# Performance work log

Measured on AMD Instinct MI355X. Metric: run time of the kernel, lower is better.

Reference implementation:

```python
import jax, jax.numpy as jnp
import numpy as np

VOCAB, EMB, UNITS, DENSE, B, T = 100, 10, 32, 25, 4096, 512

def setup_inputs() -> dict:
    key = jax.random.key(0)
    ks = jax.random.split(key, 7)
    inputs = jax.random.randint(ks[0], (B, T), 0, VOCAB, dtype=jnp.int32)
    emb = jax.random.normal(ks[1], (VOCAB, EMB), dtype=jnp.float32) * 0.05
    kernel = jax.random.normal(ks[2], (EMB, 3 * UNITS), dtype=jnp.float32) * 0.1
    rec_kernel = jax.random.normal(ks[3], (UNITS, 3 * UNITS), dtype=jnp.float32) * 0.1
    bias = jnp.zeros((2, 3 * UNITS), dtype=jnp.float32)  # [input_bias, recurrent_bias] (reset_after=True)
    dense_w = jax.random.normal(ks[4], (UNITS, DENSE), dtype=jnp.float32) * 0.1
    dense_b = jnp.zeros((DENSE,), dtype=jnp.float32)
    return {"inputs": inputs, "emb": emb, "kernel": kernel, "rec_kernel": rec_kernel,
            "bias": bias, "dense_w": dense_w, "dense_b": dense_b}

def _gru(x, kernel, rec_kernel, bias):
    # x: [B, T, EMB]. Keras GRU v2 semantics, reset_after=True, eval mode (no dropout).
    xg = jnp.einsum('bti,ij->btj', x, kernel) + bias[0]          # [B, T, 3U]
    xg = jnp.transpose(xg, (1, 0, 2))                            # [T, B, 3U]
    xz, xr, xh = jnp.split(xg, 3, axis=-1)
    h0 = jnp.zeros((x.shape[0], UNITS), dtype=x.dtype)

    def step(h, xs):
        xz_t, xr_t, xh_t = xs
        inner = h @ rec_kernel + bias[1]                         # [B, 3U]
        rz, rr, rh = jnp.split(inner, 3, axis=-1)
        z = jax.nn.sigmoid(xz_t + rz)
        r = jax.nn.sigmoid(xr_t + rr)
        hh = jnp.tanh(xh_t + r * rh)
        h_new = z * h + (1.0 - z) * hh
        return h_new, h_new

    _, hs = jax.lax.scan(step, h0, (xz, xr, xh))                 # hs: [T, B, U]
    return jnp.transpose(hs, (1, 0, 2))                          # [B, T, U]

def reference(inputs, emb, kernel, rec_kernel, bias, dense_w, dense_b):
    x = emb[inputs]                                              # [B, T, EMB]
    h = _gru(x, kernel, rec_kernel, bias)                        # [B, T, U]
    y = jax.nn.relu(jnp.einsum('btu,ud->btd', h, dense_w) + dense_b)  # [B, T, 25]
    return y.reshape(y.shape[0], -1)                             # [B, T*25]
```

## Files before the change

### kernel.cpp

```cpp
#include <hip/hip_runtime.h>

#define VOCABN 100
#define EMBN 10
#define UNITSN 32
#define DENSEN 25
#define BATCHN 4096
#define SEQN 512
#define G3 96

__device__ __forceinline__ float fast_sigmoid(float x) {
    float e = __builtin_amdgcn_exp2f(x * -1.4426950408889634f);
    return __builtin_amdgcn_rcpf(1.0f + e);
}
__device__ __forceinline__ float fast_tanh(float x) {
    float e = __builtin_amdgcn_exp2f(x * -2.8853900817779268f);
    float s = __builtin_amdgcn_rcpf(1.0f + e);
    return 2.0f * s - 1.0f;
}

__global__ __launch_bounds__(256, 2) void gru_fused_kernel(
    const int* __restrict__ inputs,
    const float* __restrict__ emb,
    const float* __restrict__ kern,
    const float* __restrict__ reck,
    const float* __restrict__ bias,
    const float* __restrict__ dw,
    const float* __restrict__ dbias,
    float* __restrict__ out)
{
    __shared__ float embP[VOCABN * G3];
    __shared__ float hbuf[8][UNITSN];
    __shared__ int   idxb[8][32];

    const int tid = threadIdx.x;

    for (int e = tid; e < VOCABN * G3; e += 256) {
        const int v = e / G3;
        const int n = e - v * G3;
        float a = bias[n];
        #pragma unroll
        for (int k = 0; k < EMBN; ++k)
            a = fmaf(emb[v * EMBN + k], kern[k * G3 + n], a);
        embP[e] = a;
    }
    __syncthreads();

    const int lane = tid & 63;
    const int wv   = tid >> 6;
    const int g    = lane >> 5;
    const int jj   = lane & 31;
    const int row  = wv * 2 + g;
    const int batch = blockIdx.x * 8 + row;

    float wz[UNITSN], wr[UNITSN], wh[UNITSN], wd[UNITSN];
    #pragma unroll
    for (int u = 0; u < UNITSN; ++u) {
        wz[u] = reck[u * G3 + jj];
        wr[u] = reck[u * G3 + 32 + jj];
        wh[u] = reck[u * G3 + 64 + jj];
    }
    #pragma unroll
    for (int u = 0; u < UNITSN; ++u)
        wd[u] = (jj < DENSEN) ? dw[u * DENSEN + jj] : 0.0f;

    const float rbz = bias[G3 + jj];
    const float rbr = bias[G3 + 32 + jj];
    const float rbh = bias[G3 + 64 + jj];
    const float dbj = (jj < DENSEN) ? dbias[jj] : 0.0f;

    const int* __restrict__ inrow  = inputs + (size_t)batch * SEQN;
    float* __restrict__     outrow = out + (size_t)batch * (size_t)(SEQN * DENSEN);

    float h[UNITSN];
    #pragma unroll
    for (int u = 0; u < UNITSN; ++u) h[u] = 0.0f;
    float hj = 0.0f;

    for (int t = 0; t < SEQN; ++t) {
        if ((t & 31) == 0) {
            idxb[row][jj] = inrow[t + jj];
        }
        const int idx = idxb[row][t & 31];
        const float* ep = embP + idx * G3;
        const float xz = ep[jj];
        const float xr = ep[32 + jj];
        const float xh = ep[64 + jj];

        float rz = rbz, rr = rbr, rh = rbh;
        #pragma unroll
        for (int u = 0; u < UNITSN; ++u) {
            rz = fmaf(h[u], wz[u], rz);
            rr = fmaf(h[u], wr[u], rr);
            rh = fmaf(h[u], wh[u], rh);
        }

        const float z  = fast_sigmoid(xz + rz);
        const float r  = fast_sigmoid(xr + rr);
        const float hh = fast_tanh(fmaf(r, rh, xh));
        hj = fmaf(z, hj - hh, hh);

        hbuf[row][jj] = hj;
        #pragma unroll
        for (int q = 0; q < 8; ++q) {
            const float4 v4 = *reinterpret_cast<const float4*>(&hbuf[row][q * 4]);
            h[q * 4 + 0] = v4.x;
            h[q * 4 + 1] = v4.y;
            h[q * 4 + 2] = v4.z;
            h[q * 4 + 3] = v4.w;
        }

        float acc = dbj;
        #pragma unroll
        for (int u = 0; u < UNITSN; ++u)
            acc = fmaf(h[u], wd[u], acc);
        if (jj < DENSEN)
            outrow[t * DENSEN + jj] = fmaxf(acc, 0.0f);
    }
}

extern "C" void kernel_launch(void* const* d_in, const int* in_sizes, int n_in,
                              void* d_out, int out_size, void* d_ws, size_t ws_size,
                              hipStream_t stream) {
    const int*   inputs = (const int*)d_in[0];
    const float* emb    = (const float*)d_in[1];
    const float* kern   = (const float*)d_in[2];
    const float* reck   = (const float*)d_in[3];
    const float* bias   = (const float*)d_in[4];
    const float* dw     = (const float*)d_in[5];
    const float* dbias  = (const float*)d_in[6];
    float* out = (float*)d_out;

    dim3 grid(BATCHN / 8);
    dim3 block(256);
    hipLaunchKernelGGL(gru_fused_kernel, grid, block, 0, stream,
                       inputs, emb, kern, reck, bias, dw, dbias, out);
}
```

Measured before the change: 484.1 us.

## Split GRU recurrent dot product across wave halves with shuffle reduction

Each batch row is now handled by a full 64-lane wavefront instead of 32 lanes. The two halves each compute a partial dot product over 16 of the 32 hidden units and combine the results with __shfl_xor. This halves the per-thread serial FMA chain and register footprint, allowing a higher occupancy target (launch bounds 4). The recurrent z/r biases are folded into the precomputed embedding projection, and token indices are loaded 64 at a time. In exchange it doubles the number of blocks and wavefronts, adds shuffle latency to every step, and duplicates the gate arithmetic in both halves.

```diff
diff --git a/kernel.cpp b/kernel.cpp
--- a/kernel.cpp
+++ b/kernel.cpp
@@ -18,7 +18,7 @@
     return 2.0f * s - 1.0f;
 }
 
-__global__ __launch_bounds__(256, 2) void gru_fused_kernel(
+__global__ __launch_bounds__(256, 4) void gru_fused_kernel(
     const int* __restrict__ inputs,
     const float* __restrict__ emb,
     const float* __restrict__ kern,
@@ -29,92 +29,94 @@
     float* __restrict__ out)
 {
     __shared__ float embP[VOCABN * G3];
-    __shared__ float hbuf[8][UNITSN];
-    __shared__ int   idxb[8][32];
+    __shared__ float hbuf[4][UNITSN];
+    __shared__ int   idxb[4][64];
 
     const int tid = threadIdx.x;
 
     for (int e = tid; e < VOCABN * G3; e += 256) {
         const int v = e / G3;
         const int n = e - v * G3;
-        float a = bias[n];
+        float a = bias[n] + ((n < 64) ? bias[G3 + n] : 0.0f);
         #pragma unroll
-        for (int k = 0; k < EMBN; ++k)
-            a = fmaf(emb[v * EMBN + k], kern[k * G3 + n], a);
+        for (int q = 0; q < EMBN; ++q)
+            a = fmaf(emb[v * EMBN + q], kern[q * G3 + n], a);
         embP[e] = a;
     }
     __syncthreads();
 
     const int lane = tid & 63;
     const int wv   = tid >> 6;
-    const int g    = lane >> 5;
+    const int k    = lane >> 5;
     const int jj   = lane & 31;
-    const int row  = wv * 2 + g;
-    const int batch = blockIdx.x * 8 + row;
+    const int u0   = k * 16;
+    const int batch = blockIdx.x * 4 + wv;
 
-    float wz[UNITSN], wr[UNITSN], wh[UNITSN], wd[UNITSN];
+    float wz[16], wr[16], wh[16], wd[16];
     #pragma unroll
-    for (int u = 0; u < UNITSN; ++u) {
-        wz[u] = reck[u * G3 + jj];
-        wr[u] = reck[u * G3 + 32 + jj];
-        wh[u] = reck[u * G3 + 64 + jj];
+    for (int i = 0; i < 16; ++i) {
+        const int u = u0 + i;
+        wz[i] = reck[u * G3 + jj];
+        wr[i] = reck[u * G3 + 32 + jj];
+        wh[i] = reck[u * G3 + 64 + jj];
+        wd[i] = (jj < DENSEN) ? dw[u * DENSEN + jj] : 0.0f;
     }
-    #pragma unroll
-    for (int u = 0; u < UNITSN; ++u)
-        wd[u] = (jj < DENSEN) ? dw[u * DENSEN + jj] : 0.0f;
-
-    const float rbz = bias[G3 + jj];
-    const float rbr = bias[G3 + 32 + jj];
-    const float rbh = bias[G3 + 64 + jj];
-    const float dbj = (jj < DENSEN) ? dbias[jj] : 0.0f;
+    const float rbh = k ? 0.0f : bias[G3 + 64 + jj];
+    const float dbj = (k == 0 && jj < DENSEN) ? dbias[jj] : 0.0f;
 
     const int* __restrict__ inrow  = inputs + (size_t)batch * SEQN;
     float* __restrict__     outrow = out + (size_t)batch * (size_t)(SEQN * DENSEN);
 
-    float h[UNITSN];
+    float h[16];
     #pragma unroll
-    for (int u = 0; u < UNITSN; ++u) h[u] = 0.0f;
+    for (int i = 0; i < 16; ++i) h[i] = 0.0f;
     float hj = 0.0f;
 
-    for (int t = 0; t < SEQN; ++t) {
-        if ((t & 31) == 0) {
-            idxb[row][jj] = inrow[t + jj];
+    for (int t0 = 0; t0 < SEQN; t0 += 64) {
+        idxb[wv][lane] = inrow[t0 + lane];
+
+        for (int tt = 0; tt < 64; ++tt) {
+            const int t = t0 + tt;
+            const int idx = idxb[wv][tt];
+            const float* ep = embP + idx * G3;
+            const float xz = ep[jj];
+            const float xr = ep[32 + jj];
+            const float xh = ep[64 + jj];
+
+            float rz = 0.0f, rr = 0.0f, rh = rbh;
+            #pragma unroll
+            for (int i = 0; i < 16; ++i) {
+                rz = fmaf(h[i], wz[i], rz);
+                rr = fmaf(h[i], wr[i], rr);
+                rh = fmaf(h[i], wh[i], rh);
+            }
+            rz += __shfl_xor(rz, 32);
+            rr += __shfl_xor(rr, 32);
+            rh += __shfl_xor(rh, 32);
+
+            const float z  = fast_sigmoid(xz + rz);
+            const float r  = fast_sigmoid(xr + rr);
+            const float hh = fast_tanh(fmaf(r, rh, xh));
+            hj = fmaf(z, hj - hh, hh);
+
+            if (k == 0) hbuf[wv][jj] = hj;
+            #pragma unroll
+            for (int q = 0; q < 4; ++q) {
+                const float4 v4 = *reinterpret_cast<const float4*>(&hbuf[wv][u0 + q * 4]);
+                h[q * 4 + 0] = v4.x;
+                h[q * 4 + 1] = v4.y;
+                h[q * 4 + 2] = v4.z;
+                h[q * 4 + 3] = v4.w;
+            }
+
+            float acc = dbj;
+            #pragma unroll
+            for (int i = 0; i < 16; ++i)
+                acc = fmaf(h[i], wd[i], acc);
+            acc += __shfl_xor(acc, 32);
+            if (k == 0 && jj < DENSEN)
+                outrow[t * DENSEN + jj] = fmaxf(acc, 0.0f);
         }
-        const int idx = idxb[row][t & 31];
-        const float* ep = embP + idx * G3;
-        const float xz = ep[jj];
-        const float xr = ep[32 + jj];
-        const float xh = ep[64 + jj];
-
-        float rz = rbz, rr = rbr, rh = rbh;
-        #pragma unroll
-        for (int u = 0; u < UNITSN; ++u) {
-            rz = fmaf(h[u], wz[u], rz);
-            rr = fmaf(h[u], wr[u], rr);
-            rh = fmaf(h[u], wh[u], rh);
-        }
-
-        const float z  = fast_sigmoid(xz + rz);
-        const float r  = fast_sigmoid(xr + rr);
-        const float hh = fast_tanh(fmaf(r, rh, xh));
-        hj = fmaf(z, hj - hh, hh);
-
-        hbuf[row][jj] = hj;
-        #pragma unroll
-        for (int q = 0; q < 8; ++q) {
-            const float4 v4 = *reinterpret_cast<const float4*>(&hbuf[row][q * 4]);
-            h[q * 4 + 0] = v4.x;
-            h[q * 4 + 1] = v4.y;
-            h[q * 4 + 2] = v4.z;
-            h[q * 4 + 3] = v4.w;
-        }
-
-        float acc = dbj;
-        #pragma unroll
-        for (int u = 0; u < UNITSN; ++u)
-            acc = fmaf(h[u], wd[u], acc);
-        if (jj < DENSEN)
-            outrow[t * DENSEN + jj] = fmaxf(acc, 0.0f);
     }
 }
 
@@ -130,7 +132,7 @@
     const float* dbias  = (const float*)d_in[6];
     float* out = (float*)d_out;
 
-    dim3 grid(BATCHN / 8);
+    dim3 grid(BATCHN / 4);
     dim3 block(256);
     hipLaunchKernelGGL(gru_fused_kernel, grid, block, 0, stream,
                        inputs, emb, kern, reck, bias, dw, dbias, out);
```

Result: slower. 523.3 us (+8.1%).
